# Kernel optimization log

Hardware: AMD Instinct MI355X
Metric: run time of the kernel (lower is better)

The kernel has to match this reference:

```python
import jax, jax.numpy as jnp
import numpy as np

B, D_IN, D, C = 64, 1024, 768, 1000
EPS = 0.1        # args.alpha_cap
NUM_SIM = 3      # args.num_sim


def setup_inputs() -> dict:
    key = jax.random.key(0)
    k0, k1, k2, k3 = jax.random.split(key, 4)
    return {
        "x": jax.random.normal(k0, (B, D_IN), jnp.float32),
        "W_emb": jax.random.normal(k1, (D, D_IN), jnp.float32) * 0.02,
        "b_emb": jnp.zeros((D,), jnp.float32),
        "W_fc": jax.random.normal(k2, (C, D), jnp.float32) * 0.02,
        "b_fc": jnp.zeros((C,), jnp.float32),
        "anchors": jax.random.normal(k3, (C, D), jnp.float32),
    }


def _forward_core(x, W_emb, b_emb, W_fc, b_fc, anchors):
    # self.embedding(x): feature extractor -> [B, D]
    emb = x @ W_emb.T + b_emb
    # self.model(x) head logits -> [B, C]
    logits = emb @ W_fc.T + b_fc
    # compute_ulb_grads: grad of CE(fc(emb), onehot_j) wrt emb = (softmax - onehot_j) @ W_fc.
    # softmax is shared across all pseudo-labels j, so grad_ij = G_i - W_fc[j].
    p = jax.nn.softmax(logits, axis=-1)          # [B, C]
    G = p @ W_fc                                  # [B, D]
    grads = G[:, None, :] - W_fc[None, :, :]      # [B, C, D]
    # calculate_optimum_alpha: z = anchor - ulb_embed
    z = anchors[None, :, :] - emb[:, None, :]     # [B, C, D]
    z_norm = jnp.linalg.norm(z, axis=-1, keepdims=True)        # [B, C, 1]
    g_norm = jnp.linalg.norm(grads, axis=-1, keepdims=True)    # [B, C, 1]
    alpha = (EPS * z_norm / g_norm) * grads / (z + 1e-8)       # [B, C, D]
    # mix_feature: (1-alpha)*ulb_embed + alpha*anchor
    mix = (1.0 - alpha) * emb[:, None, :] + alpha * anchors[None, :, :]  # [B, C, D]
    # fc(feature_mix) -> [B, C, C]
    logits_mix = jnp.einsum('bjd,cd->bjc', mix, W_fc) + b_fc
    return logits, logits_mix


def reference(x, W_emb, b_emb, W_fc, b_fc, anchors):
    logits, logits_mix = _forward_core(x, W_emb, b_emb, W_fc, b_fc, anchors)
    predictions = jnp.argmax(logits, axis=-1)       # [B]
    preds_mix = jnp.argmax(logits_mix, axis=-1)     # [B, C]
    counts = jnp.zeros((B, C), jnp.float32)
    counts = counts.at[jnp.arange(B), predictions].add(1.0)
    counts = counts.at[jnp.arange(B)[:, None], preds_mix].add(1.0)
    # all_below_threshold: labels_count < num_sample everywhere
    return jnp.all(counts < NUM_SIM, axis=1)
```

## Files before the change

kernel.cpp:

```cpp
#include <hip/hip_runtime.h>
#include <stdint.h>
#include <stddef.h>

#define BB 64
#define DIN 1024
#define DD 768
#define CC 1000
#define EPSA 0.1f
#define NSIM 3

typedef short  s16x8 __attribute__((ext_vector_type(8)));
typedef float  f32x4 __attribute__((ext_vector_type(4)));

static __device__ __forceinline__ unsigned short f2bf_rne(float x) {
  unsigned u = __float_as_uint(x);
  return (unsigned short)((u + 0x7FFFu + ((u >> 16) & 1u)) >> 16);
}
static __device__ __forceinline__ float bf2f(unsigned short h) {
  return __uint_as_float(((unsigned)h) << 16);
}

__global__ __launch_bounds__(256) void prep_kernel(const float* __restrict__ W_fc,
                                                   const float* __restrict__ anchors,
                                                   const float* __restrict__ W_emb,
                                                   const float* __restrict__ x,
                                                   short* __restrict__ Bp, short* __restrict__ Ap,
                                                   short* __restrict__ Ip, short* __restrict__ Xp,
                                                   float* __restrict__ An2) {
  const int blk = blockIdx.x, tid = threadIdx.x;
  if (blk < 1184) {
    const float* src; short* dst; int KS, nrow, gid;
    if (blk < 384)       { src = W_fc;    dst = Bp; KS = 24; nrow = CC;  gid = blk * 256 + tid; }
    else if (blk < 768)  { src = anchors; dst = Ap; KS = 24; nrow = CC;  gid = (blk - 384) * 256 + tid; }
    else if (blk < 1152) { src = W_emb;   dst = Ip; KS = 32; nrow = DD;  gid = (blk - 768) * 256 + tid; }
    else                 { src = x;       dst = Xp; KS = 32; nrow = BB;  gid = (blk - 1152) * 256 + tid; }
    int lane = gid & 63;
    int ks   = (gid >> 6) % KS;
    int nt   = gid / (64 * KS);
    int row  = nt * 16 + (lane & 15);
    int k0   = ks * 32 + (lane >> 4) * 8;
    int stride = KS * 32;
    s16x8 v;
    #pragma unroll
    for (int r = 0; r < 8; ++r) {
      float w = (row < nrow) ? src[(size_t)row * stride + k0 + r] : 0.0f;
      v[r] = (short)f2bf_rne(w);
    }
    ((s16x8*)dst)[gid] = v;
  } else {
    int w = tid >> 6, lane = tid & 63;
    int j = (blk - 1184) * 4 + w;
    const float4* ar = (const float4*)(anchors + (size_t)j * DD);
    float an = 0.f;
    for (int k4 = lane; k4 < DD / 4; k4 += 64) {
      float4 a = ar[k4];
      an += a.x*a.x + a.y*a.y + a.z*a.z + a.w*a.w;
    }
    #pragma unroll
    for (int o = 1; o < 64; o <<= 1) an += __shfl_xor(an, o);
    if (lane == 0) An2[j] = an;
  }
}

__global__ __launch_bounds__(256) void embV_kernel(const short* __restrict__ Bp,
                                                   const short* __restrict__ Ip,
                                                   const short* __restrict__ Xp,
                                                   const float* __restrict__ b_emb,
                                                   unsigned short* __restrict__ Vb,
                                                   float* __restrict__ emb) {
  const int tid = threadIdx.x, w = tid >> 6, lane = tid & 63;
  if (blockIdx.x < 256) {
    const int bx = blockIdx.x & 15, cb = blockIdx.x >> 4;
    const int rnt = bx * 4 + w;
    const s16x8* BH = (const s16x8*)Bp;
    f32x4 acc[4] = {};
    for (int ks = 0; ks < 24; ++ks) {
      s16x8 a = BH[(rnt * 24 + ks) * 64 + lane];
      #pragma unroll
      for (int nf = 0; nf < 4; ++nf)
        acc[nf] = __builtin_amdgcn_mfma_f32_16x16x32_bf16(a, BH[((cb * 4 + nf) * 24 + ks) * 64 + lane], acc[nf], 0, 0, 0);
    }
    const int r0 = rnt * 16 + (lane >> 4) * 4;
    const int c0 = cb * 64 + (lane & 15);
    #pragma unroll
    for (int nf = 0; nf < 4; ++nf)
      #pragma unroll
      for (int rr = 0; rr < 4; ++rr)
        Vb[(size_t)(r0 + rr) * 1024 + c0 + nf * 16] = f2bf_rne(acc[nf][rr]);
  } else {
    const int g = blockIdx.x - 256;
    const int nfr = g * 4 + w;
    const s16x8* XH = (const s16x8*)Xp;
    const s16x8* IH = (const s16x8*)Ip;
    f32x4 acc[4] = {};
    for (int ks = 0; ks < 32; ++ks) {
      s16x8 b = IH[(nfr * 32 + ks) * 64 + lane];
      #pragma unroll
      for (int mt = 0; mt < 4; ++mt)
        acc[mt] = __builtin_amdgcn_mfma_f32_16x16x32_bf16(XH[(mt * 32 + ks) * 64 + lane], b, acc[mt], 0, 0, 0);
    }
    const int d = nfr * 16 + (lane & 15);
    const float be = b_emb[d];
    #pragma unroll
    for (int mt = 0; mt < 4; ++mt)
      #pragma unroll
      for (int rr = 0; rr < 4; ++rr)
        emb[(size_t)(mt * 16 + (lane >> 4) * 4 + rr) * DD + d] = acc[mt][rr] + be;
  }
}

__global__ __launch_bounds__(256) void packmid_kernel(const unsigned short* __restrict__ Vb,
                                                      const float* __restrict__ emb,
                                                      short* __restrict__ Vp,
                                                      short* __restrict__ Ep) {
  const int blk = blockIdx.x, tid = threadIdx.x;
  if (blk < 512) {
    int gid = blk * 256 + tid;
    int lane = gid & 63, ks = (gid >> 6) % 32, nt = gid / (64 * 32);
    int row = nt * 16 + (lane & 15);
    int k0  = ks * 32 + (lane >> 4) * 8;
    ((s16x8*)Vp)[gid] = *(const s16x8*)(Vb + (size_t)row * 1024 + k0);
  } else {
    int gid = (blk - 512) * 256 + tid;
    if (gid >= 4 * 24 * 64) return;
    int lane = gid & 63, ks = (gid >> 6) % 24, mt = gid / (64 * 24);
    int row = mt * 16 + (lane & 15);
    int k0  = ks * 32 + (lane >> 4) * 8;
    s16x8 v;
    #pragma unroll
    for (int r = 0; r < 8; ++r) v[r] = (short)f2bf_rne(emb[(size_t)row * DD + k0 + r]);
    ((s16x8*)Ep)[gid] = v;
  }
}

__global__ __launch_bounds__(64) void logitsAE_kernel(const short* __restrict__ Ep,
                                                      const short* __restrict__ Bp,
                                                      const short* __restrict__ Ap,
                                                      const float* __restrict__ b_fc,
                                                      float* __restrict__ logits,
                                                      float* __restrict__ AE) {
  const int nfr = blockIdx.x;
  const int mt  = blockIdx.y;
  const int lane = threadIdx.x;
  const s16x8* E = (const s16x8*)Ep;
  const s16x8* B = (const s16x8*)Bp;
  const s16x8* A = (const s16x8*)Ap;
  f32x4 accL = {}, accA = {};
  for (int ks = 0; ks < 24; ++ks) {
    s16x8 a  = E[(mt * 24 + ks) * 64 + lane];
    s16x8 bW = B[(nfr * 24 + ks) * 64 + lane];
    s16x8 bA = A[(nfr * 24 + ks) * 64 + lane];
    accL = __builtin_amdgcn_mfma_f32_16x16x32_bf16(a, bW, accL, 0, 0, 0);
    accA = __builtin_amdgcn_mfma_f32_16x16x32_bf16(a, bA, accA, 0, 0, 0);
  }
  const int c = nfr * 16 + (lane & 15);
  if (c < CC) {
    const float bf = b_fc[c];
    #pragma unroll
    for (int rr = 0; rr < 4; ++rr) {
      int b = mt * 16 + (lane >> 4) * 4 + rr;
      logits[b * CC + c] = accL[rr] + bf;
      AE[b * CC + c]     = accA[rr];
    }
  }
}

__global__ __launch_bounds__(256) void softmax_kernel(const float* __restrict__ logits,
                                                      const float* __restrict__ emb,
                                                      float* __restrict__ p,
                                                      short* __restrict__ Pp,
                                                      int* __restrict__ pred,
                                                      float* __restrict__ En2) {
  int b = blockIdx.x, t = threadIdx.x;
  __shared__ float smax[256];
  __shared__ int   sidx[256];
  __shared__ float ssum[256];
  {
    float pe = 0.f;
    for (int k = t; k < DD; k += 256) { float e = emb[b * DD + k]; pe += e * e; }
    #pragma unroll
    for (int o = 1; o < 64; o <<= 1) pe += __shfl_xor(pe, o);
    __shared__ float se[4];
    if ((t & 63) == 0) se[t >> 6] = pe;
    __syncthreads();
    if (t == 0) En2[b] = se[0] + se[1] + se[2] + se[3];
  }
  float m = -3.402823466e38f; int mi = 0;
  for (int c = t; c < CC; c += 256) {
    float v = logits[b * CC + c];
    if (v > m) { m = v; mi = c; }
  }
  smax[t] = m; sidx[t] = mi;
  __syncthreads();
  for (int o = 128; o > 0; o >>= 1) {
    if (t < o) {
      float v2 = smax[t + o]; int i2 = sidx[t + o];
      if (v2 > smax[t] || (v2 == smax[t] && i2 < sidx[t])) { smax[t] = v2; sidx[t] = i2; }
    }
    __syncthreads();
  }
  float M = smax[0];
  if (t == 0) pred[b] = sidx[0];
  float sum = 0.f;
  for (int c = t; c < CC; c += 256) sum += expf(logits[b * CC + c] - M);
  ssum[t] = sum;
  __syncthreads();
  for (int o = 128; o > 0; o >>= 1) {
    if (t < o) ssum[t] += ssum[t + o];
    __syncthreads();
  }
  float S = ssum[0];
  const int mt = b >> 4, blo = b & 15;
  for (int j = t; j < CC; j += 256) {
    float pj = expf(logits[b * CC + j] - M) / S;
    p[b * CC + j] = pj;
    size_t fi = ((size_t)(mt * 32 + (j >> 5)) * 64 + ((j >> 3) & 3) * 16 + blo) * 8 + (j & 7);
    Pp[fi] = (short)f2bf_rne(pj);
  }
  if (t < 24) {
    int j = 1000 + t;
    size_t fi = ((size_t)(mt * 32 + (j >> 5)) * 64 + ((j >> 3) & 3) * 16 + blo) * 8 + (j & 7);
    Pp[fi] = 0;
  }
}

__global__ __launch_bounds__(64) void u_kernel(const short* __restrict__ Pp,
                                               const short* __restrict__ Vp,
                                               float* __restrict__ u) {
  const int nfr = blockIdx.x;
  const int mt  = blockIdx.y;
  const int lane = threadIdx.x;
  const s16x8* P = (const s16x8*)Pp;
  const s16x8* V = (const s16x8*)Vp;
  f32x4 acc = {};
  for (int ks = 0; ks < 32; ++ks) {
    s16x8 b = V[(nfr * 32 + ks) * 64 + lane];
    acc = __builtin_amdgcn_mfma_f32_16x16x32_bf16(P[(mt * 32 + ks) * 64 + lane], b, acc, 0, 0, 0);
  }
  const int c = nfr * 16 + (lane & 15);
  if (c < CC) {
    #pragma unroll
    for (int rr = 0; rr < 4; ++rr)
      u[(mt * 16 + (lane >> 4) * 4 + rr) * CC + c] = acc[rr];
  }
}

__global__ __launch_bounds__(256) void scan_kernel(const float* __restrict__ logits,
                                                   const float* __restrict__ u,
                                                   const float* __restrict__ p,
                                                   const float* __restrict__ AE,
                                                   const float* __restrict__ An2,
                                                   const float* __restrict__ En2,
                                                   const unsigned short* __restrict__ Vb,
                                                   int* __restrict__ pm) {
  const int b = blockIdx.x, jb = blockIdx.y;
  const int tid = threadIdx.x, w = tid >> 6, lane = tid & 63;
  const int c0 = lane * 16;

  float L[16], U[16];
  float part = 0.f;
  #pragma unroll
  for (int g = 0; g < 4; ++g) {
    int cg = c0 + g * 4;
    if (cg + 3 < CC) {
      float4 l4 = *(const float4*)(logits + b * CC + cg);
      float4 u4 = *(const float4*)(u + b * CC + cg);
      float4 p4 = *(const float4*)(p + b * CC + cg);
      L[g*4+0]=l4.x; L[g*4+1]=l4.y; L[g*4+2]=l4.z; L[g*4+3]=l4.w;
      U[g*4+0]=u4.x; U[g*4+1]=u4.y; U[g*4+2]=u4.z; U[g*4+3]=u4.w;
      part += p4.x*u4.x + p4.y*u4.y + p4.z*u4.z + p4.w*u4.w;
    } else {
      #pragma unroll
      for (int i2 = 0; i2 < 4; ++i2) {
        int c = cg + i2;
        bool ok = (c < CC);
        float lv = ok ? logits[b * CC + c] : -3.402823466e38f;
        float uv = ok ? u[b * CC + c] : 0.f;
        float pv = ok ? p[b * CC + c] : 0.f;
        L[g*4+i2] = lv; U[g*4+i2] = uv;
        part += pv * uv;
      }
    }
  }
  #pragma unroll
  for (int o = 1; o < 64; o <<= 1) part += __shfl_xor(part, o);
  const float gn2b = part;
  const float en2 = En2[b];

  for (int jj = 0; jj < 8; ++jj) {
    int j = jb * 32 + w * 8 + jj;
    if (j >= CC) break;
    float zn2 = An2[j] - 2.0f * AE[b * CC + j] + en2;
    float gn2 = gn2b - 2.0f * u[b * CC + j] + bf2f(Vb[(size_t)j * 1024 + j]);
    float sj = (EPSA * sqrtf(zn2)) / sqrtf(gn2);
    const s16x8* Vr = (const s16x8*)(Vb + (size_t)j * 1024);
    s16x8 v8a = Vr[lane * 2];
    s16x8 v8b = Vr[lane * 2 + 1];
    float best = -3.402823466e38f; int bi = 0;
    #pragma unroll
    for (int i = 0; i < 8; ++i) {
      float v = bf2f((unsigned short)v8a[i]);
      float val = L[i] + sj * (U[i] - v);
      if (val > best) { best = val; bi = c0 + i; }
    }
    #pragma unroll
    for (int i = 0; i < 8; ++i) {
      float v = bf2f((unsigned short)v8b[i]);
      float val = L[8 + i] + sj * (U[8 + i] - v);
      if (val > best) { best = val; bi = c0 + 8 + i; }
    }
    #pragma unroll
    for (int o = 1; o < 64; o <<= 1) {
      float ov = __shfl_xor(best, o);
      int   oi = __shfl_xor(bi, o);
      if (ov > best || (ov == best && oi < bi)) { best = ov; bi = oi; }
    }
    if (lane == 0) pm[b * CC + j] = bi;
  }
}

__global__ __launch_bounds__(256) void counts_kernel(const int* __restrict__ pm,
                                                     const int* __restrict__ pred,
                                                     float* __restrict__ out) {
  int b = blockIdx.x, t = threadIdx.x;
  __shared__ int cnt[CC];
  __shared__ int bad;
  for (int c = t; c < CC; c += 256) cnt[c] = 0;
  if (t == 0) bad = 0;
  __syncthreads();
  if (t == 0) atomicAdd(&cnt[pred[b]], 1);
  for (int j = t; j < CC; j += 256) atomicAdd(&cnt[pm[b * CC + j]], 1);
  __syncthreads();
  for (int c = t; c < CC; c += 256) if (cnt[c] >= NSIM) bad = 1;
  __syncthreads();
  if (t == 0) out[b] = bad ? 0.0f : 1.0f;
}

extern "C" void kernel_launch(void* const* d_in, const int* in_sizes, int n_in,
                              void* d_out, int out_size, void* d_ws, size_t ws_size,
                              hipStream_t stream) {
  const float* x       = (const float*)d_in[0];
  const float* W_emb   = (const float*)d_in[1];
  const float* b_emb   = (const float*)d_in[2];
  const float* W_fc    = (const float*)d_in[3];
  const float* b_fc    = (const float*)d_in[4];
  const float* anchors = (const float*)d_in[5];
  float* out = (float*)d_out;

  float* emb    = (float*)d_ws;
  float* logits = emb + BB * DD;
  float* p      = logits + BB * CC;
  float* u      = p + BB * CC;
  float* AE     = u + BB * CC;
  float* An2    = AE + BB * CC;
  float* En2    = An2 + 1024;
  int*   pred   = (int*)(En2 + 64);
  int*   pm     = pred + 64;
  short* Bp     = (short*)(pm + BB * CC);
  short* Ap     = Bp + 64 * 24 * 64 * 8;
  short* Ip     = Ap + 64 * 24 * 64 * 8;
  short* Xp     = Ip + 48 * 32 * 64 * 8;
  short* Ep     = Xp + 4 * 32 * 64 * 8;
  short* Pp     = Ep + 4 * 24 * 64 * 8;
  unsigned short* Vb = (unsigned short*)(Pp + 4 * 32 * 64 * 8);
  short* Vp     = (short*)(Vb + 1024 * 1024);

  hipLaunchKernelGGL(prep_kernel,    dim3(1434), dim3(256), 0, stream,
                     W_fc, anchors, W_emb, x, Bp, Ap, Ip, Xp, An2);
  hipLaunchKernelGGL(embV_kernel,    dim3(268), dim3(256), 0, stream, Bp, Ip, Xp, b_emb, Vb, emb);
  hipLaunchKernelGGL(packmid_kernel, dim3(536), dim3(256), 0, stream, Vb, emb, Vp, Ep);
  hipLaunchKernelGGL(logitsAE_kernel,dim3(64, 4), dim3(64), 0, stream, Ep, Bp, Ap, b_fc, logits, AE);
  hipLaunchKernelGGL(softmax_kernel, dim3(BB), dim3(256), 0, stream, logits, emb, p, Pp, pred, En2);
  hipLaunchKernelGGL(u_kernel,       dim3(64, 4), dim3(64), 0, stream, Pp, Vp, u);
  hipLaunchKernelGGL(scan_kernel,    dim3(BB, 32), dim3(256), 0, stream,
                     logits, u, p, AE, An2, En2, Vb, pm);
  hipLaunchKernelGGL(counts_kernel,  dim3(BB), dim3(256), 0, stream, pm, pred, out);
}
```

Baseline: 87.45 us.

## Batch four pseudo-labels per wave in scan kernel and double grid

The scan kernel now handles 4 labels per wave instead of 8. It issues all V-row loads up front, computes the four scale factors together, and interleaves the four argmax shuffle reductions so their latencies overlap. The grid's y dimension doubles to keep coverage, which gives more parallelism. The cost is more registers and a repeated per-block prologue (loading logits and u and reducing the dot product) across twice as many blocks.

```diff
diff --git a/kernel.cpp b/kernel.cpp
--- a/kernel.cpp
+++ b/kernel.cpp
@@ -256,6 +256,7 @@
   const int b = blockIdx.x, jb = blockIdx.y;
   const int tid = threadIdx.x, w = tid >> 6, lane = tid & 63;
   const int c0 = lane * 16;
+  const int jbase = jb * 16 + w * 4;
 
   float L[16], U[16];
   float part = 0.f;
@@ -287,35 +288,55 @@
   const float gn2b = part;
   const float en2 = En2[b];
 
-  for (int jj = 0; jj < 8; ++jj) {
-    int j = jb * 32 + w * 8 + jj;
-    if (j >= CC) break;
-    float zn2 = An2[j] - 2.0f * AE[b * CC + j] + en2;
-    float gn2 = gn2b - 2.0f * u[b * CC + j] + bf2f(Vb[(size_t)j * 1024 + j]);
-    float sj = (EPSA * sqrtf(zn2)) / sqrtf(gn2);
-    const s16x8* Vr = (const s16x8*)(Vb + (size_t)j * 1024);
-    s16x8 v8a = Vr[lane * 2];
-    s16x8 v8b = Vr[lane * 2 + 1];
-    float best = -3.402823466e38f; int bi = 0;
+  int jr[4];
+  s16x8 va[4], vbh[4];
+  #pragma unroll
+  for (int jj = 0; jj < 4; ++jj) {
+    int j = jbase + jj;
+    jr[jj] = (j < CC) ? j : (CC - 1);
+    const s16x8* Vr = (const s16x8*)(Vb + (size_t)jr[jj] * 1024);
+    va[jj]  = Vr[lane * 2];
+    vbh[jj] = Vr[lane * 2 + 1];
+  }
+  float sj[4];
+  #pragma unroll
+  for (int jj = 0; jj < 4; ++jj) {
+    float zn2 = An2[jr[jj]] - 2.0f * AE[b * CC + jr[jj]] + en2;
+    float gn2 = gn2b - 2.0f * u[b * CC + jr[jj]] + bf2f(Vb[(size_t)jr[jj] * 1024 + jr[jj]]);
+    sj[jj] = (EPSA * sqrtf(zn2)) / sqrtf(gn2);
+  }
+  float best[4]; int bi[4];
+  #pragma unroll
+  for (int jj = 0; jj < 4; ++jj) {
+    float bst = -3.402823466e38f; int bix = 0;
     #pragma unroll
     for (int i = 0; i < 8; ++i) {
-      float v = bf2f((unsigned short)v8a[i]);
-      float val = L[i] + sj * (U[i] - v);
-      if (val > best) { best = val; bi = c0 + i; }
+      float val = L[i] + sj[jj] * (U[i] - bf2f((unsigned short)va[jj][i]));
+      if (val > bst) { bst = val; bix = c0 + i; }
     }
     #pragma unroll
     for (int i = 0; i < 8; ++i) {
-      float v = bf2f((unsigned short)v8b[i]);
-      float val = L[8 + i] + sj * (U[8 + i] - v);
-      if (val > best) { best = val; bi = c0 + 8 + i; }
-    }
-    #pragma unroll
-    for (int o = 1; o < 64; o <<= 1) {
-      float ov = __shfl_xor(best, o);
-      int   oi = __shfl_xor(bi, o);
-      if (ov > best || (ov == best && oi < bi)) { best = ov; bi = oi; }
-    }
-    if (lane == 0) pm[b * CC + j] = bi;
+      float val = L[8 + i] + sj[jj] * (U[8 + i] - bf2f((unsigned short)vbh[jj][i]));
+      if (val > bst) { bst = val; bix = c0 + 8 + i; }
+    }
+    best[jj] = bst; bi[jj] = bix;
+  }
+  #pragma unroll
+  for (int o = 1; o < 64; o <<= 1) {
+    float ov[4]; int oi[4];
+    #pragma unroll
+    for (int jj = 0; jj < 4; ++jj) { ov[jj] = __shfl_xor(best[jj], o); oi[jj] = __shfl_xor(bi[jj], o); }
+    #pragma unroll
+    for (int jj = 0; jj < 4; ++jj) {
+      if (ov[jj] > best[jj] || (ov[jj] == best[jj] && oi[jj] < bi[jj])) { best[jj] = ov[jj]; bi[jj] = oi[jj]; }
+    }
+  }
+  if (lane == 0) {
+    #pragma unroll
+    for (int jj = 0; jj < 4; ++jj) {
+      int j = jbase + jj;
+      if (j < CC) pm[b * CC + j] = bi[jj];
+    }
   }
 }
 
@@ -372,7 +393,7 @@
   hipLaunchKernelGGL(logitsAE_kernel,dim3(64, 4), dim3(64), 0, stream, Ep, Bp, Ap, b_fc, logits, AE);
   hipLaunchKernelGGL(softmax_kernel, dim3(BB), dim3(256), 0, stream, logits, emb, p, Pp, pred, En2);
   hipLaunchKernelGGL(u_kernel,       dim3(64, 4), dim3(64), 0, stream, Pp, Vp, u);
-  hipLaunchKernelGGL(scan_kernel,    dim3(BB, 32), dim3(256), 0, stream,
+  hipLaunchKernelGGL(scan_kernel,    dim3(BB, 64), dim3(256), 0, stream,
                      logits, u, p, AE, An2, En2, Vb, pm);
   hipLaunchKernelGGL(counts_kernel,  dim3(BB), dim3(256), 0, stream, pm, pred, out);
 }
```

Result: no change. 86.27 us (-1.4%).

## Restructure argmax scan: thread-per-label over class chunks with packed-key cross-block max

Applied to the files above, without the earlier changes.

The scan kernel no longer uses one wave per pseudo-label j with a 64-lane shuffle argmax. Each thread now owns four labels j and loops serially over a 125-class chunk, with logits and u staged in shared memory. Per-chunk partial maxima are written as packed 64-bit order-preserving keys that encode both value and index, and the counts kernel reduces them across the 8 chunks. This removes the per-j shuffle reductions and reads Vb column-wise. The cost is an extra 4MB partial buffer and strided 8-byte loads from Vb.

```diff
diff --git a/kernel.cpp b/kernel.cpp
--- a/kernel.cpp
+++ b/kernel.cpp
@@ -252,74 +252,97 @@
                                                    const float* __restrict__ An2,
                                                    const float* __restrict__ En2,
                                                    const unsigned short* __restrict__ Vb,
-                                                   int* __restrict__ pm) {
-  const int b = blockIdx.x, jb = blockIdx.y;
-  const int tid = threadIdx.x, w = tid >> 6, lane = tid & 63;
-  const int c0 = lane * 16;
-
-  float L[16], U[16];
-  float part = 0.f;
-  #pragma unroll
-  for (int g = 0; g < 4; ++g) {
-    int cg = c0 + g * 4;
+                                                   unsigned long long* __restrict__ part) {
+  const int b = blockIdx.x, cz = blockIdx.y;
+  const int tid = threadIdx.x;
+  const int c0 = cz * 125;
+  __shared__ __attribute__((aligned(8))) float2 LU[128];
+  __shared__ float se[4];
+
+  if (tid < 125) {
+    int c = c0 + tid;
+    LU[tid] = float2{logits[b * CC + c], u[b * CC + c]};
+  }
+  float partsum = 0.f;
+  {
+    int cg = tid * 4;
     if (cg + 3 < CC) {
-      float4 l4 = *(const float4*)(logits + b * CC + cg);
+      float4 p4 = *(const float4*)(p + b * CC + cg);
       float4 u4 = *(const float4*)(u + b * CC + cg);
-      float4 p4 = *(const float4*)(p + b * CC + cg);
-      L[g*4+0]=l4.x; L[g*4+1]=l4.y; L[g*4+2]=l4.z; L[g*4+3]=l4.w;
-      U[g*4+0]=u4.x; U[g*4+1]=u4.y; U[g*4+2]=u4.z; U[g*4+3]=u4.w;
-      part += p4.x*u4.x + p4.y*u4.y + p4.z*u4.z + p4.w*u4.w;
+      partsum = p4.x*u4.x + p4.y*u4.y + p4.z*u4.z + p4.w*u4.w;
     } else {
       #pragma unroll
-      for (int i2 = 0; i2 < 4; ++i2) {
-        int c = cg + i2;
-        bool ok = (c < CC);
-        float lv = ok ? logits[b * CC + c] : -3.402823466e38f;
-        float uv = ok ? u[b * CC + c] : 0.f;
-        float pv = ok ? p[b * CC + c] : 0.f;
-        L[g*4+i2] = lv; U[g*4+i2] = uv;
-        part += pv * uv;
+      for (int i = 0; i < 4; ++i) {
+        int c = cg + i;
+        if (c < CC) partsum += p[b * CC + c] * u[b * CC + c];
       }
     }
   }
   #pragma unroll
-  for (int o = 1; o < 64; o <<= 1) part += __shfl_xor(part, o);
-  const float gn2b = part;
+  for (int o = 1; o < 64; o <<= 1) partsum += __shfl_xor(partsum, o);
+  if ((tid & 63) == 0) se[tid >> 6] = partsum;
+  __syncthreads();
+  const float gn2b = se[0] + se[1] + se[2] + se[3];
   const float en2 = En2[b];
 
-  for (int jj = 0; jj < 8; ++jj) {
-    int j = jb * 32 + w * 8 + jj;
-    if (j >= CC) break;
-    float zn2 = An2[j] - 2.0f * AE[b * CC + j] + en2;
-    float gn2 = gn2b - 2.0f * u[b * CC + j] + bf2f(Vb[(size_t)j * 1024 + j]);
-    float sj = (EPSA * sqrtf(zn2)) / sqrtf(gn2);
-    const s16x8* Vr = (const s16x8*)(Vb + (size_t)j * 1024);
-    s16x8 v8a = Vr[lane * 2];
-    s16x8 v8b = Vr[lane * 2 + 1];
-    float best = -3.402823466e38f; int bi = 0;
-    #pragma unroll
-    for (int i = 0; i < 8; ++i) {
-      float v = bf2f((unsigned short)v8a[i]);
-      float val = L[i] + sj * (U[i] - v);
-      if (val > best) { best = val; bi = c0 + i; }
-    }
-    #pragma unroll
-    for (int i = 0; i < 8; ++i) {
-      float v = bf2f((unsigned short)v8b[i]);
-      float val = L[8 + i] + sj * (U[8 + i] - v);
-      if (val > best) { best = val; bi = c0 + 8 + i; }
-    }
-    #pragma unroll
-    for (int o = 1; o < 64; o <<= 1) {
-      float ov = __shfl_xor(best, o);
-      int   oi = __shfl_xor(bi, o);
-      if (ov > best || (ov == best && oi < bi)) { best = ov; bi = oi; }
-    }
-    if (lane == 0) pm[b * CC + j] = bi;
-  }
-}
-
-__global__ __launch_bounds__(256) void counts_kernel(const int* __restrict__ pm,
+  const int jt = (tid < 250 ? tid : 249) * 4;
+  float4 an4 = *(const float4*)(An2 + jt);
+  float4 ae4 = *(const float4*)(AE + b * CC + jt);
+  float4 uj4 = *(const float4*)(u + b * CC + jt);
+  float sj[4], nsj[4];
+  {
+    float anv[4] = {an4.x, an4.y, an4.z, an4.w};
+    float aev[4] = {ae4.x, ae4.y, ae4.z, ae4.w};
+    float ujv[4] = {uj4.x, uj4.y, uj4.z, uj4.w};
+    #pragma unroll
+    for (int k = 0; k < 4; ++k) {
+      float vd  = bf2f(Vb[(size_t)(jt + k) * 1024 + jt + k]);
+      float zn2 = anv[k] - 2.0f * aev[k] + en2;
+      float gn2 = gn2b - 2.0f * ujv[k] + vd;
+      sj[k] = (EPSA * sqrtf(zn2)) / sqrtf(gn2);
+      nsj[k] = -sj[k];
+    }
+  }
+
+  float best[4] = {-3.402823466e38f, -3.402823466e38f, -3.402823466e38f, -3.402823466e38f};
+  int   bi[4]   = {0, 0, 0, 0};
+  const unsigned short* Vcol = Vb + jt;
+  #pragma unroll 5
+  for (int i = 0; i < 125; ++i) {
+    int c = c0 + i;
+    float2 lu = LU[i];
+    uint2 vv = *(const uint2*)(Vcol + (size_t)c * 1024);
+    float v0 = __uint_as_float(vv.x << 16);
+    float v1 = __uint_as_float(vv.x & 0xffff0000u);
+    float v2 = __uint_as_float(vv.y << 16);
+    float v3 = __uint_as_float(vv.y & 0xffff0000u);
+    float t0 = fmaf(sj[0], lu.y, lu.x);
+    float t1 = fmaf(sj[1], lu.y, lu.x);
+    float t2 = fmaf(sj[2], lu.y, lu.x);
+    float t3 = fmaf(sj[3], lu.y, lu.x);
+    float val0 = fmaf(nsj[0], v0, t0);
+    float val1 = fmaf(nsj[1], v1, t1);
+    float val2 = fmaf(nsj[2], v2, t2);
+    float val3 = fmaf(nsj[3], v3, t3);
+    if (val0 > best[0]) { best[0] = val0; bi[0] = c; }
+    if (val1 > best[1]) { best[1] = val1; bi[1] = c; }
+    if (val2 > best[2]) { best[2] = val2; bi[2] = c; }
+    if (val3 > best[3]) { best[3] = val3; bi[3] = c; }
+  }
+
+  if (tid < 250) {
+    unsigned long long* dst = part + (size_t)cz * 64000 + b * 1000 + jt;
+    #pragma unroll
+    for (int k = 0; k < 4; ++k) {
+      unsigned ub = __float_as_uint(best[k]);
+      ub = (ub & 0x80000000u) ? ~ub : (ub | 0x80000000u);
+      dst[k] = ((unsigned long long)ub << 32) |
+               (unsigned long long)(0xFFFFFFFFu - (unsigned)bi[k]);
+    }
+  }
+}
+
+__global__ __launch_bounds__(256) void counts_kernel(const unsigned long long* __restrict__ part,
                                                      const int* __restrict__ pred,
                                                      float* __restrict__ out) {
   int b = blockIdx.x, t = threadIdx.x;
@@ -329,7 +352,17 @@
   if (t == 0) bad = 0;
   __syncthreads();
   if (t == 0) atomicAdd(&cnt[pred[b]], 1);
-  for (int j = t; j < CC; j += 256) atomicAdd(&cnt[pm[b * CC + j]], 1);
+  const unsigned long long* pr = part + b * 1000;
+  for (int j = t; j < CC; j += 256) {
+    unsigned long long key = 0;
+    #pragma unroll
+    for (int cz = 0; cz < 8; ++cz) {
+      unsigned long long k2 = pr[(size_t)cz * 64000 + j];
+      key = (k2 > key) ? k2 : key;
+    }
+    int c = (int)(0xFFFFFFFFu - (unsigned)(key & 0xFFFFFFFFull));
+    atomicAdd(&cnt[c], 1);
+  }
   __syncthreads();
   for (int c = t; c < CC; c += 256) if (cnt[c] >= NSIM) bad = 1;
   __syncthreads();
@@ -355,8 +388,8 @@
   float* An2    = AE + BB * CC;
   float* En2    = An2 + 1024;
   int*   pred   = (int*)(En2 + 64);
-  int*   pm     = pred + 64;
-  short* Bp     = (short*)(pm + BB * CC);
+  unsigned long long* part = (unsigned long long*)(pred + 64);
+  short* Bp     = (short*)(part + 8 * 64000);
   short* Ap     = Bp + 64 * 24 * 64 * 8;
   short* Ip     = Ap + 64 * 24 * 64 * 8;
   short* Xp     = Ip + 48 * 32 * 64 * 8;
@@ -372,7 +405,7 @@
   hipLaunchKernelGGL(logitsAE_kernel,dim3(64, 4), dim3(64), 0, stream, Ep, Bp, Ap, b_fc, logits, AE);
   hipLaunchKernelGGL(softmax_kernel, dim3(BB), dim3(256), 0, stream, logits, emb, p, Pp, pred, En2);
   hipLaunchKernelGGL(u_kernel,       dim3(64, 4), dim3(64), 0, stream, Pp, Vp, u);
-  hipLaunchKernelGGL(scan_kernel,    dim3(BB, 32), dim3(256), 0, stream,
-                     logits, u, p, AE, An2, En2, Vb, pm);
-  hipLaunchKernelGGL(counts_kernel,  dim3(BB), dim3(256), 0, stream, pm, pred, out);
-}
+  hipLaunchKernelGGL(scan_kernel,    dim3(BB, 8), dim3(256), 0, stream,
+                     logits, u, p, AE, An2, En2, Vb, part);
+  hipLaunchKernelGGL(counts_kernel,  dim3(BB), dim3(256), 0, stream, part, pred, out);
+}
```

Measured after the change: 73.19 us. 1.19x faster.
